# Kernel optimization log

Measured on AMD Instinct MI355X. Metric: run time of the kernel, lower is better.

The kernel has to match this reference:

```python
import jax, jax.numpy as jnp
import numpy as np

N_NODES = 100000
N_EDGES = 3200000
N_GRAPHS = 4096
N_REL = 5
N_BASES = 4
HID = 32


def setup_inputs() -> dict:
    key = jax.random.key(0)
    ks = jax.random.split(key, 32)
    inp = {}
    inp['x'] = jax.random.normal(ks[0], (N_NODES, 4), dtype=jnp.float32)
    inp['edge_index'] = jax.random.randint(ks[1], (2, N_EDGES), 0, N_NODES, dtype=jnp.int64)
    inp['edge_type'] = jax.random.randint(ks[2], (N_EDGES,), 0, N_REL, dtype=jnp.int64)
    inp['user_idx'] = jax.random.randint(ks[3], (N_GRAPHS,), 0, N_NODES, dtype=jnp.int64)
    inp['item_idx'] = jax.random.randint(ks[4], (N_GRAPHS,), 0, N_NODES, dtype=jnp.int64)
    k = 5
    for l in range(4):
        in_c = 4 if l == 0 else HID
        inp[f'basis{l}'] = jax.random.normal(ks[k], (N_BASES, in_c, HID), dtype=jnp.float32) * 0.1; k += 1
        inp[f'comp{l}'] = jax.random.normal(ks[k], (N_REL, N_BASES), dtype=jnp.float32) * 0.5; k += 1
        inp[f'root{l}'] = jax.random.normal(ks[k], (in_c, HID), dtype=jnp.float32) * 0.1; k += 1
        inp[f'bias{l}'] = jax.random.normal(ks[k], (HID,), dtype=jnp.float32) * 0.01; k += 1
    inp['w1'] = jax.random.normal(ks[k], (256, 128), dtype=jnp.float32) * 0.05; k += 1
    inp['b1'] = jnp.zeros((128,), dtype=jnp.float32)
    inp['w2'] = jax.random.normal(ks[k], (128, 1), dtype=jnp.float32) * 0.05; k += 1
    inp['b2'] = jnp.zeros((1,), dtype=jnp.float32)
    return inp


def _rgcn_layer(x, src, key5, inv_cnt, basis, comp, root, bias, n_nodes):
    # mean-aggregate raw source features per (dst, relation): [N, R, in]
    agg = jax.ops.segment_sum(x[src], key5, num_segments=n_nodes * N_REL)
    agg = agg.reshape(n_nodes, N_REL, -1) * inv_cnt
    # basis-decomposed relation weights: W_r = sum_b comp[r,b] * basis[b]
    w = jnp.einsum('rb,bio->rio', comp, basis)  # [R, in, out]
    return jnp.einsum('nri,rio->no', agg, w) + x @ root + bias


def reference(x, edge_index, edge_type, user_idx, item_idx,
              basis0, comp0, root0, bias0,
              basis1, comp1, root1, bias1,
              basis2, comp2, root2, bias2,
              basis3, comp3, root3, bias3,
              w1, b1, w2, b2):
    n_nodes = x.shape[0]
    src, dst = edge_index[0], edge_index[1]
    key5 = dst * N_REL + edge_type  # combined (dst, relation) segment id
    cnt = jax.ops.segment_sum(jnp.ones_like(edge_type, dtype=x.dtype), key5,
                              num_segments=n_nodes * N_REL)
    inv_cnt = (1.0 / jnp.maximum(cnt, 1.0)).reshape(n_nodes, N_REL, 1)
    params = [(basis0, comp0, root0, bias0), (basis1, comp1, root1, bias1),
              (basis2, comp2, root2, bias2), (basis3, comp3, root3, bias3)]
    out = x
    hs = []
    for (basis, comp, root, bias) in params:
        out = jnp.tanh(_rgcn_layer(out, src, key5, inv_cnt, basis, comp, root, bias, n_nodes))
        hs.append(out)
    h = jnp.concatenate(hs, axis=1)            # [N, 128]
    g = jnp.concatenate([h[user_idx], h[item_idx]], axis=1)  # [B, 256]
    z = jax.nn.relu(g @ w1 + b1)
    return (z @ w2 + b2)[:, 0]
```

## Files before the change

### kernel.cpp

```cpp
#include <hip/hip_runtime.h>
#include <hip/hip_bf16.h>
#include <hip/hip_fp16.h>

#define N_NODES 100000
#define N_EDGES 3200000
#define N_GRAPHS 4096
#define N_REL 5
#define N_BASES 4
#define HID 32
#define SEG (N_NODES*N_REL)
#define DUMMY N_NODES

#define NBUCK 392
#define BCAP  10240
#define PBCAP 15360
#define NKEY  1280
#define PTILE 4096

#define KDIM 192
#define ASTR 208

typedef _Float16 half8 __attribute__((ext_vector_type(8)));
typedef float floatx4 __attribute__((ext_vector_type(4)));

static __global__ __launch_bounds__(256) void k_part(const int* __restrict__ ei,
                                                     const int* __restrict__ et,
                                                     int* __restrict__ gcur,
                                                     unsigned long long* __restrict__ part) {
    __shared__ unsigned long long stage[PTILE];
    __shared__ int hist[NBUCK];
    __shared__ int lofs[NBUCK];
    __shared__ int lbase[NBUCK];
    __shared__ int sscan[256];
    int t = threadIdx.x;
    int e0 = blockIdx.x * PTILE;
    int tile_n = N_EDGES - e0; if (tile_n > PTILE) tile_n = PTILE;

    for (int k = t; k < NBUCK; k += 256) hist[k] = 0;
    __syncthreads();
    int src[16], bkt[16], lkey[16];
#pragma unroll
    for (int j = 0; j < 16; j++) {
        int e = e0 + j * 256 + t;
        if (e < N_EDGES) {
            int s = ei[e];
            int d = ei[N_EDGES + e];
            int r = et[e];
            src[j] = s; bkt[j] = d >> 8; lkey[j] = ((d & 255) * 5) + r;
            atomicAdd(&hist[bkt[j]], 1);
        } else bkt[j] = -1;
    }
    __syncthreads();
    int h0 = (2 * t     < NBUCK) ? hist[2 * t]     : 0;
    int h1 = (2 * t + 1 < NBUCK) ? hist[2 * t + 1] : 0;
    int s2 = h0 + h1;
    sscan[t] = s2;
    __syncthreads();
    for (int off = 1; off < 256; off <<= 1) {
        int xv = (t >= off) ? sscan[t - off] : 0;
        __syncthreads();
        sscan[t] += xv;
        __syncthreads();
    }
    int excl = sscan[t] - s2;
    if (2 * t     < NBUCK) lofs[2 * t]     = excl;
    if (2 * t + 1 < NBUCK) lofs[2 * t + 1] = excl + h0;
    for (int k = t; k < NBUCK; k += 256) lbase[k] = atomicAdd(&gcur[k], hist[k]);
    __syncthreads();
    for (int k = t; k < NBUCK; k += 256) hist[k] = 0;
    __syncthreads();
#pragma unroll
    for (int j = 0; j < 16; j++) {
        if (bkt[j] >= 0) {
            int rank = atomicAdd(&hist[bkt[j]], 1);
            stage[lofs[bkt[j]] + rank] =
                ((unsigned long long)(unsigned)((bkt[j] << 16) | lkey[j]) << 32)
                | (unsigned)src[j];
        }
    }
    __syncthreads();
    for (int i = t; i < tile_n; i += 256) {
        unsigned long long u = stage[i];
        unsigned hi = (unsigned)(u >> 32);
        int bb = hi >> 16;
        unsigned long long lk = hi & 0xFFFFu;
        int pos = lbase[bb] + (i - lofs[bb]);
        if (pos < BCAP)
            part[(size_t)bb * BCAP + pos] = (lk << 32) | (u & 0xffffffffULL);
    }
}

static __global__ __launch_bounds__(1024) void k_bsort(const unsigned long long* __restrict__ part,
                                                       const int* __restrict__ gcur,
                                                       int* __restrict__ offs,
                                                       int* __restrict__ cnt,
                                                       int* __restrict__ srcs) {
    __shared__ int lhist[NKEY];
    __shared__ int lscan[NKEY];
    __shared__ int sscan[256];
    __shared__ int lsrc[PBCAP];
    int b = blockIdx.x;
    int t = threadIdx.x;
    int n = gcur[b]; if (n > BCAP) n = BCAP;
    const unsigned long long* reg = part + (size_t)b * BCAP;

    for (int k = t; k < NKEY; k += 1024) lhist[k] = 0;
    __syncthreads();
    for (int i = t; i < n; i += 1024)
        atomicAdd(&lhist[(int)(reg[i] >> 32)], 1);
    __syncthreads();

    int loc[5]; int s5 = 0;
    if (t < 256) {
#pragma unroll
        for (int j = 0; j < 5; j++) { loc[j] = s5; s5 += (lhist[t * 5 + j] + 7) & ~7; }
        sscan[t] = s5;
    }
    __syncthreads();
    for (int off = 1; off < 256; off <<= 1) {
        int x = (t >= off && t < 256) ? sscan[t - off] : 0;
        __syncthreads();
        if (t < 256) sscan[t] += x;
        __syncthreads();
    }
    if (t < 256) {
        int excl = sscan[t] - s5;
#pragma unroll
        for (int j = 0; j < 5; j++) lscan[t * 5 + j] = excl + loc[j];
    }
    __syncthreads();
    int ptot = sscan[255]; if (ptot > PBCAP) ptot = PBCAP;
    int pout = ptot + 16; if (pout > PBCAP) pout = PBCAP;

    int base = b * PBCAP;
    if (t < 256) {
#pragma unroll
        for (int j = 0; j < 5; j++) {
            int k = t * 5 + j;
            int segid = b * NKEY + k;
            if (segid < SEG) {
                cnt[segid]  = lhist[k];
                offs[segid] = base + lscan[k];
            }
        }
    }
    __syncthreads();
    for (int k = t; k < NKEY; k += 1024) lhist[k] = 0;
    for (int i = t; i < pout; i += 1024) lsrc[i] = DUMMY;
    __syncthreads();
    for (int i = t; i < n; i += 1024) {
        unsigned long long u = reg[i];
        int k = (int)(u >> 32);
        int pos = lscan[k] + atomicAdd(&lhist[k], 1);
        if (pos < PBCAP) lsrc[pos] = (int)(u & 0xffffffffULL);
    }
    __syncthreads();
    for (int i = t; i < pout; i += 1024) srcs[base + i] = lsrc[i];
}

static __global__ __launch_bounds__(256) void k_prep(
    const float* __restrict__ x,
    __half* __restrict__ ht0, __half* __restrict__ ht1, __half* __restrict__ ht2,
    __half* __restrict__ ht3, __half* __restrict__ ht4, int* __restrict__ srcs,
    const float* __restrict__ ba0, const float* __restrict__ co0, const float* __restrict__ ro0,
    const float* __restrict__ ba1, const float* __restrict__ co1, const float* __restrict__ ro1,
    const float* __restrict__ ba2, const float* __restrict__ co2, const float* __restrict__ ro2,
    const float* __restrict__ ba3, const float* __restrict__ co3, const float* __restrict__ ro3,
    __half* __restrict__ Wb, const float* __restrict__ w1, __half* __restrict__ Wm) {
    int blk = blockIdx.x;
    int t = threadIdx.x;
    if (blk < 12501) {
        int tid = blk * 256 + t;
        if (tid < (N_NODES + 1) * 32) {
            int nd = tid >> 5, ii = tid & 31;
            float v = (nd < N_NODES && ii < 4) ? x[(nd << 2) + ii] : 0.f;
            ht0[tid] = __float2half(v);
        } else {
            int r = tid - (N_NODES + 1) * 32;
            if (r < 128) {
                __half* hp = (r < 32) ? ht1 : (r < 64) ? ht2 : (r < 96) ? ht3 : ht4;
                hp[N_NODES * 32 + (r & 31)] = __float2half(0.f);
            } else if (r < 144) srcs[NBUCK * PBCAP + (r - 128)] = DUMMY;
        }
    } else if (blk < 12501 + 96) {
        int idx = (blk - 12501) * 256 + t;
        int j    = idx & 7;
        int lane = (idx >> 3) & 63;
        int tile = (idx >> 9) & 1;
        int ls   = idx >> 10;
        int l    = ls / 6;
        int s    = ls - l * 6;
        const float* basis = (l == 0) ? ba0 : (l == 1) ? ba1 : (l == 2) ? ba2 : ba3;
        const float* comp  = (l == 0) ? co0 : (l == 1) ? co1 : (l == 2) ? co2 : co3;
        const float* root  = (l == 0) ? ro0 : (l == 1) ? ro1 : (l == 2) ? ro2 : ro3;
        int in_c = (l == 0) ? 4 : HID;
        int d = ((lane >> 4) << 3) + j;
        int o = tile * 16 + (lane & 15);
        float v = 0.f;
        if (d < in_c) {
            if (s < 5) {
                float acc = 0.f;
#pragma unroll
                for (int b = 0; b < N_BASES; b++)
                    acc += comp[s * N_BASES + b] * basis[(b * in_c + d) * HID + o];
                v = acc;
            } else {
                v = root[d * HID + o];
            }
        }
        Wb[idx] = __float2half(v);
    } else {
        int idx = (blk - 12597) * 256 + t;
        int j    = idx & 7;
        int lane = (idx >> 3) & 63;
        int s    = (idx >> 9) & 7;
        int tile = idx >> 12;
        int k = s * 32 + ((lane >> 4) << 3) + j;
        int o = tile * 16 + (lane & 15);
        Wm[idx] = __float2half(w1[k * 128 + o]);
    }
}

static __global__ __launch_bounds__(128, 5) void k_layer(
    const __half* __restrict__ tab, const int* __restrict__ offs,
    const int* __restrict__ cnt, const int* __restrict__ srcs,
    const __half* __restrict__ Wbl, const float* __restrict__ bias,
    __half* __restrict__ hout) {
    __shared__ __align__(16) __half sAgg[32 * ASTR];
    int t = threadIdx.x;
    int wave = t >> 6, lane = t & 63;
    int nsub = lane >> 2, cp = lane & 3;
    int nl = wave * 16 + nsub;
    int n = blockIdx.x * 32 + nl;
    const half8* tab8 = (const half8*)tab;

    int s5 = n * N_REL;
    int o0 = offs[s5];
    int cc[5];
#pragma unroll
    for (int r = 0; r < 5; r++) cc[r] = cnt[s5 + r];

    __half* row = sAgg + nl * ASTR;
    *(half8*)(row + 160 + cp * 8) = tab8[n * 4 + cp];

    int ob[5];
    {
        int orun = o0;
#pragma unroll
        for (int r = 0; r < 5; r++) { ob[r] = orun; orun += (cc[r] + 7) & ~7; }
    }
    int4 E0[5], E1[5];
#pragma unroll
    for (int r = 0; r < 5; r++) {
        const int* sp = srcs + ob[r];
        E0[r] = *(const int4*)(sp);
        E1[r] = *(const int4*)(sp + 4);
    }
#pragma unroll
    for (int r = 0; r < 5; r++) {
        int cr = cc[r];
        int pr = (cr + 7) & ~7;
        const int* sp = srcs + ob[r];
        half8 g0 = tab8[E0[r].x * 4 + cp], g1 = tab8[E0[r].y * 4 + cp];
        half8 g2 = tab8[E0[r].z * 4 + cp], g3 = tab8[E0[r].w * 4 + cp];
        half8 g4 = tab8[E1[r].x * 4 + cp], g5 = tab8[E1[r].y * 4 + cp];
        half8 g6 = tab8[E1[r].z * 4 + cp], g7 = tab8[E1[r].w * 4 + cp];
        half8 sb = ((g0 + g1) + (g2 + g3)) + ((g4 + g5) + (g6 + g7));
        float S0 = (float)sb[0], S1 = (float)sb[1], S2 = (float)sb[2], S3 = (float)sb[3];
        float S4 = (float)sb[4], S5 = (float)sb[5], S6 = (float)sb[6], S7 = (float)sb[7];
        for (int s8 = 8; s8 < pr; s8 += 8) {
            int4 f0 = *(const int4*)(sp + s8);
            int4 f1 = *(const int4*)(sp + s8 + 4);
            half8 h0 = tab8[f0.x * 4 + cp], h1 = tab8[f0.y * 4 + cp];
            half8 h2 = tab8[f0.z * 4 + cp], h3 = tab8[f0.w * 4 + cp];
            half8 h4 = tab8[f1.x * 4 + cp], h5 = tab8[f1.y * 4 + cp];
            half8 h6 = tab8[f1.z * 4 + cp], h7 = tab8[f1.w * 4 + cp];
            half8 rb = ((h0 + h1) + (h2 + h3)) + ((h4 + h5) + (h6 + h7));
            S0 += (float)rb[0]; S1 += (float)rb[1]; S2 += (float)rb[2]; S3 += (float)rb[3];
            S4 += (float)rb[4]; S5 += (float)rb[5]; S6 += (float)rb[6]; S7 += (float)rb[7];
        }
        float ic = (cr > 0) ? __builtin_amdgcn_rcpf((float)cr) : 0.f;
        half8 u;
        u[0] = (_Float16)(S0 * ic); u[1] = (_Float16)(S1 * ic);
        u[2] = (_Float16)(S2 * ic); u[3] = (_Float16)(S3 * ic);
        u[4] = (_Float16)(S4 * ic); u[5] = (_Float16)(S5 * ic);
        u[6] = (_Float16)(S6 * ic); u[7] = (_Float16)(S7 * ic);
        *(half8*)(row + r * 32 + cp * 8) = u;
    }
    __syncthreads();

    floatx4 acc0 = {0.f, 0.f, 0.f, 0.f}, acc1 = {0.f, 0.f, 0.f, 0.f};
    const __half* aBase = sAgg + (wave * 16 + (lane & 15)) * ASTR + ((lane >> 4) << 3);
    const __half* bBase = Wbl + lane * 8;
#pragma unroll
    for (int s = 0; s < 6; s++) {
        half8 a  = *(const half8*)(aBase + s * 32);
        half8 f0 = *(const half8*)(bBase + (s * 2 + 0) * 512);
        half8 f1 = *(const half8*)(bBase + (s * 2 + 1) * 512);
        acc0 = __builtin_amdgcn_mfma_f32_16x16x32_f16(a, f0, acc0, 0, 0, 0);
        acc1 = __builtin_amdgcn_mfma_f32_16x16x32_f16(a, f1, acc1, 0, 0, 0);
    }
    int oc = lane & 15;
    float bi0 = bias[oc], bi1 = bias[16 + oc];
#pragma unroll
    for (int r = 0; r < 4; r++) {
        int node = blockIdx.x * 32 + wave * 16 + ((lane >> 4) << 2) + r;
        hout[node * 32 + oc]      = __float2half(tanhf(acc0[r] + bi0));
        hout[node * 32 + 16 + oc] = __float2half(tanhf(acc1[r] + bi1));
    }
}

static __global__ __launch_bounds__(256) void k_mlp(
    const __half* __restrict__ h1, const __half* __restrict__ h2,
    const __half* __restrict__ h3, const __half* __restrict__ h4,
    const int* __restrict__ uidx, const int* __restrict__ iidx,
    const __half* __restrict__ Wm, const float* __restrict__ b1,
    const float* __restrict__ w2, const float* __restrict__ b2,
    float* __restrict__ out) {
    __shared__ __align__(16) __half sg[16 * 264];
    __shared__ float sacc[4][16];
    int t = threadIdx.x, wave = t >> 6, lane = t & 63;
    int g0 = blockIdx.x * 16;
    int lt = lane >> 4, lp = lane & 15;
    const __half* htab = (lt == 0) ? h1 : (lt == 1) ? h2 : (lt == 2) ? h3 : h4;
#pragma unroll
    for (int gg2 = 0; gg2 < 4; gg2++) {
        int gg = wave * 4 + gg2;
        int g = g0 + gg;
        int u = uidx[g], it = iidx[g];
        __half2* dst = (__half2*)(sg + gg * 264);
        dst[lt * 16 + lp]      = ((const __half2*)(htab + u * 32))[lp];
        dst[64 + lt * 16 + lp] = ((const __half2*)(htab + it * 32))[lp];
    }
    __syncthreads();
    floatx4 acc0 = {0.f, 0.f, 0.f, 0.f}, acc1 = {0.f, 0.f, 0.f, 0.f};
    const __half* aBase = sg + (lane & 15) * 264 + ((lane >> 4) << 3);
    const __half* bB0 = Wm + (wave * 2 + 0) * 4096 + lane * 8;
    const __half* bB1 = Wm + (wave * 2 + 1) * 4096 + lane * 8;
#pragma unroll
    for (int s = 0; s < 8; s++) {
        half8 a  = *(const half8*)(aBase + s * 32);
        half8 f0 = *(const half8*)(bB0 + s * 512);
        half8 f1 = *(const half8*)(bB1 + s * 512);
        acc0 = __builtin_amdgcn_mfma_f32_16x16x32_f16(a, f0, acc0, 0, 0, 0);
        acc1 = __builtin_amdgcn_mfma_f32_16x16x32_f16(a, f1, acc1, 0, 0, 0);
    }
    int o0 = wave * 32 + (lane & 15);
    int o1 = o0 + 16;
    float b10 = b1[o0], b11 = b1[o1], w20 = w2[o0], w21 = w2[o1];
#pragma unroll
    for (int r = 0; r < 4; r++) {
        float z0 = fmaxf(acc0[r] + b10, 0.f);
        float z1 = fmaxf(acc1[r] + b11, 0.f);
        float v = z0 * w20 + z1 * w21;
#pragma unroll
        for (int off = 1; off < 16; off <<= 1) v += __shfl_xor(v, off);
        if ((lane & 15) == 0) sacc[wave][((lane >> 4) << 2) + r] = v;
    }
    __syncthreads();
    if (t < 16)
        out[g0 + t] = sacc[0][t] + sacc[1][t] + sacc[2][t] + sacc[3][t] + b2[0];
}

extern "C" void kernel_launch(void* const* d_in, const int* in_sizes, int n_in,
                              void* d_out, int out_size, void* d_ws, size_t ws_size,
                              hipStream_t stream) {
    const float* x  = (const float*)d_in[0];
    const int*   ei = (const int*)d_in[1];
    const int*   et = (const int*)d_in[2];
    const int*   ui = (const int*)d_in[3];
    const int*   ii = (const int*)d_in[4];
    const float* w1 = (const float*)d_in[21];
    const float* b1 = (const float*)d_in[22];
    const float* w2 = (const float*)d_in[23];
    const float* b2 = (const float*)d_in[24];

    char* ws = (char*)d_ws;
    if (ws_size < 92167680UL) return;
    int*    gcur = (int*)(ws + 0);
    int*    offs = (int*)(ws + 2048);
    int*    cnt  = (int*)(ws + 2002176);
    int*    srcs = (int*)(ws + 4002304);
    __half* Wb   = (__half*)(ws + 28086912);
    __half* Wm   = (__half*)(ws + 28136064);
    __half* ht0  = (__half*)(ws + 28201600);
    __half* ht1  = (__half*)(ws + 34601728);
    __half* ht2  = (__half*)(ws + 41001856);
    __half* ht3  = (__half*)(ws + 47401984);
    __half* ht4  = (__half*)(ws + 53802112);
    unsigned long long* part = (unsigned long long*)(ws + 34601728);

    hipMemsetAsync(gcur, 0, NBUCK * 4, stream);

    k_part<<<(N_EDGES + PTILE - 1) / PTILE, 256, 0, stream>>>(ei, et, gcur, part);
    k_bsort<<<NBUCK, 1024, 0, stream>>>(part, gcur, offs, cnt, srcs);
    k_prep<<<12725, 256, 0, stream>>>(
        x, ht0, ht1, ht2, ht3, ht4, srcs,
        (const float*)d_in[5],  (const float*)d_in[6],  (const float*)d_in[7],
        (const float*)d_in[9],  (const float*)d_in[10], (const float*)d_in[11],
        (const float*)d_in[13], (const float*)d_in[14], (const float*)d_in[15],
        (const float*)d_in[17], (const float*)d_in[18], (const float*)d_in[19],
        Wb, w1, Wm);

    __half* tabs[5] = {ht0, ht1, ht2, ht3, ht4};
    for (int l = 0; l < 4; l++) {
        const float* bias = (const float*)d_in[8 + 4 * l];
        k_layer<<<N_NODES / 32, 128, 0, stream>>>(
            tabs[l], offs, cnt, srcs, Wb + l * 6144, bias, tabs[l + 1]);
    }
    k_mlp<<<256, 256, 0, stream>>>(ht1, ht2, ht3, ht4, ui, ii, Wm, b1, w2, b2,
                                   (float*)d_out);
}
```

Measured before the change: 335.5 us.

## Replace bucketed LDS partition sort with global atomic counting sort

```diff
diff --git a/kernel.cpp b/kernel.cpp
--- a/kernel.cpp
+++ b/kernel.cpp
@@ -8,14 +8,12 @@
 #define N_REL 5
 #define N_BASES 4
 #define HID 32
-#define SEG (N_NODES*N_REL)
+#define NKEYS (N_NODES*N_REL)
 #define DUMMY N_NODES
 
-#define NBUCK 392
-#define BCAP  10240
-#define PBCAP 15360
-#define NKEY  1280
-#define PTILE 4096
+#define SCANB 489
+#define SRCCAP 6803456
+#define FILLB 1661
 
 #define KDIM 192
 #define ASTR 208
@@ -23,145 +21,121 @@
 typedef _Float16 half8 __attribute__((ext_vector_type(8)));
 typedef float floatx4 __attribute__((ext_vector_type(4)));
 
-static __global__ __launch_bounds__(256) void k_part(const int* __restrict__ ei,
+static __global__ __launch_bounds__(256) void k_hist(const int* __restrict__ ei,
                                                      const int* __restrict__ et,
-                                                     int* __restrict__ gcur,
-                                                     unsigned long long* __restrict__ part) {
-    __shared__ unsigned long long stage[PTILE];
-    __shared__ int hist[NBUCK];
-    __shared__ int lofs[NBUCK];
-    __shared__ int lbase[NBUCK];
-    __shared__ int sscan[256];
-    int t = threadIdx.x;
-    int e0 = blockIdx.x * PTILE;
-    int tile_n = N_EDGES - e0; if (tile_n > PTILE) tile_n = PTILE;
-
-    for (int k = t; k < NBUCK; k += 256) hist[k] = 0;
-    __syncthreads();
-    int src[16], bkt[16], lkey[16];
-#pragma unroll
-    for (int j = 0; j < 16; j++) {
-        int e = e0 + j * 256 + t;
-        if (e < N_EDGES) {
-            int s = ei[e];
-            int d = ei[N_EDGES + e];
-            int r = et[e];
-            src[j] = s; bkt[j] = d >> 8; lkey[j] = ((d & 255) * 5) + r;
-            atomicAdd(&hist[bkt[j]], 1);
-        } else bkt[j] = -1;
-    }
-    __syncthreads();
-    int h0 = (2 * t     < NBUCK) ? hist[2 * t]     : 0;
-    int h1 = (2 * t + 1 < NBUCK) ? hist[2 * t + 1] : 0;
-    int s2 = h0 + h1;
-    sscan[t] = s2;
+                                                     int* __restrict__ cnt) {
+    int e = (blockIdx.x * 256 + threadIdx.x) * 4;
+    int4 d4 = *(const int4*)(ei + N_EDGES + e);
+    int4 r4 = *(const int4*)(et + e);
+    atomicAdd(&cnt[d4.x * 5 + r4.x], 1);
+    atomicAdd(&cnt[d4.y * 5 + r4.y], 1);
+    atomicAdd(&cnt[d4.z * 5 + r4.z], 1);
+    atomicAdd(&cnt[d4.w * 5 + r4.w], 1);
+}
+
+static __global__ __launch_bounds__(256) void k_scanA(const int* __restrict__ cnt,
+                                                      int* __restrict__ offs,
+                                                      int* __restrict__ bsum) {
+    __shared__ int ss[256];
+    int t = threadIdx.x;
+    int base = blockIdx.x * 1024 + t * 4;
+    int p0 = 0, p1 = 0, p2 = 0, p3 = 0;
+    if (base + 3 < NKEYS) {
+        int4 c = *(const int4*)(cnt + base);
+        p0 = (c.x + 7) & ~7; p1 = (c.y + 7) & ~7;
+        p2 = (c.z + 7) & ~7; p3 = (c.w + 7) & ~7;
+    } else {
+        if (base     < NKEYS) p0 = (cnt[base]     + 7) & ~7;
+        if (base + 1 < NKEYS) p1 = (cnt[base + 1] + 7) & ~7;
+        if (base + 2 < NKEYS) p2 = (cnt[base + 2] + 7) & ~7;
+        if (base + 3 < NKEYS) p3 = (cnt[base + 3] + 7) & ~7;
+    }
+    int s = p0 + p1 + p2 + p3;
+    ss[t] = s;
     __syncthreads();
     for (int off = 1; off < 256; off <<= 1) {
-        int xv = (t >= off) ? sscan[t - off] : 0;
+        int x = (t >= off) ? ss[t - off] : 0;
         __syncthreads();
-        sscan[t] += xv;
+        ss[t] += x;
         __syncthreads();
     }
-    int excl = sscan[t] - s2;
-    if (2 * t     < NBUCK) lofs[2 * t]     = excl;
-    if (2 * t + 1 < NBUCK) lofs[2 * t + 1] = excl + h0;
-    for (int k = t; k < NBUCK; k += 256) lbase[k] = atomicAdd(&gcur[k], hist[k]);
-    __syncthreads();
-    for (int k = t; k < NBUCK; k += 256) hist[k] = 0;
-    __syncthreads();
-#pragma unroll
-    for (int j = 0; j < 16; j++) {
-        if (bkt[j] >= 0) {
-            int rank = atomicAdd(&hist[bkt[j]], 1);
-            stage[lofs[bkt[j]] + rank] =
-                ((unsigned long long)(unsigned)((bkt[j] << 16) | lkey[j]) << 32)
-                | (unsigned)src[j];
+    int excl = ss[t] - s;
+    if (base     < NKEYS) offs[base]     = excl;
+    if (base + 1 < NKEYS) offs[base + 1] = excl + p0;
+    if (base + 2 < NKEYS) offs[base + 2] = excl + p0 + p1;
+    if (base + 3 < NKEYS) offs[base + 3] = excl + p0 + p1 + p2;
+    if (t == 255) bsum[blockIdx.x] = ss[255];
+}
+
+static __global__ __launch_bounds__(512) void k_scanB(int* __restrict__ bsum) {
+    __shared__ int ss[512];
+    int t = threadIdx.x;
+    int v = (t < SCANB) ? bsum[t] : 0;
+    ss[t] = v;
+    __syncthreads();
+    for (int off = 1; off < 512; off <<= 1) {
+        int x = (t >= off) ? ss[t - off] : 0;
+        __syncthreads();
+        ss[t] += x;
+        __syncthreads();
+    }
+    if (t < SCANB) bsum[t] = ss[t] - v;
+}
+
+static __global__ __launch_bounds__(256) void k_scanC(int* __restrict__ offs,
+                                                      const int* __restrict__ bsum,
+                                                      int* __restrict__ cur,
+                                                      int* __restrict__ srcs) {
+    int blk = blockIdx.x;
+    int t = threadIdx.x;
+    if (blk < SCANB) {
+        int bb = bsum[blk];
+        int base = blk * 1024 + t * 4;
+        if (base + 3 < NKEYS) {
+            int4 o = *(const int4*)(offs + base);
+            o.x += bb; o.y += bb; o.z += bb; o.w += bb;
+            *(int4*)(offs + base) = o;
+            *(int4*)(cur + base) = o;
+        } else {
+            for (int i = 0; i < 4; i++)
+                if (base + i < NKEYS) {
+                    int o = offs[base + i] + bb;
+                    offs[base + i] = o;
+                    cur[base + i] = o;
+                }
         }
-    }
-    __syncthreads();
-    for (int i = t; i < tile_n; i += 256) {
-        unsigned long long u = stage[i];
-        unsigned hi = (unsigned)(u >> 32);
-        int bb = hi >> 16;
-        unsigned long long lk = hi & 0xFFFFu;
-        int pos = lbase[bb] + (i - lofs[bb]);
-        if (pos < BCAP)
-            part[(size_t)bb * BCAP + pos] = (lk << 32) | (u & 0xffffffffULL);
-    }
-}
-
-static __global__ __launch_bounds__(1024) void k_bsort(const unsigned long long* __restrict__ part,
-                                                       const int* __restrict__ gcur,
-                                                       int* __restrict__ offs,
-                                                       int* __restrict__ cnt,
-                                                       int* __restrict__ srcs) {
-    __shared__ int lhist[NKEY];
-    __shared__ int lscan[NKEY];
-    __shared__ int sscan[256];
-    __shared__ int lsrc[PBCAP];
-    int b = blockIdx.x;
-    int t = threadIdx.x;
-    int n = gcur[b]; if (n > BCAP) n = BCAP;
-    const unsigned long long* reg = part + (size_t)b * BCAP;
-
-    for (int k = t; k < NKEY; k += 1024) lhist[k] = 0;
-    __syncthreads();
-    for (int i = t; i < n; i += 1024)
-        atomicAdd(&lhist[(int)(reg[i] >> 32)], 1);
-    __syncthreads();
-
-    int loc[5]; int s5 = 0;
-    if (t < 256) {
-#pragma unroll
-        for (int j = 0; j < 5; j++) { loc[j] = s5; s5 += (lhist[t * 5 + j] + 7) & ~7; }
-        sscan[t] = s5;
-    }
-    __syncthreads();
-    for (int off = 1; off < 256; off <<= 1) {
-        int x = (t >= off && t < 256) ? sscan[t - off] : 0;
-        __syncthreads();
-        if (t < 256) sscan[t] += x;
-        __syncthreads();
-    }
-    if (t < 256) {
-        int excl = sscan[t] - s5;
-#pragma unroll
-        for (int j = 0; j < 5; j++) lscan[t * 5 + j] = excl + loc[j];
-    }
-    __syncthreads();
-    int ptot = sscan[255]; if (ptot > PBCAP) ptot = PBCAP;
-    int pout = ptot + 16; if (pout > PBCAP) pout = PBCAP;
-
-    int base = b * PBCAP;
-    if (t < 256) {
-#pragma unroll
-        for (int j = 0; j < 5; j++) {
-            int k = t * 5 + j;
-            int segid = b * NKEY + k;
-            if (segid < SEG) {
-                cnt[segid]  = lhist[k];
-                offs[segid] = base + lscan[k];
-            }
-        }
-    }
-    __syncthreads();
-    for (int k = t; k < NKEY; k += 1024) lhist[k] = 0;
-    for (int i = t; i < pout; i += 1024) lsrc[i] = DUMMY;
-    __syncthreads();
-    for (int i = t; i < n; i += 1024) {
-        unsigned long long u = reg[i];
-        int k = (int)(u >> 32);
-        int pos = lscan[k] + atomicAdd(&lhist[k], 1);
-        if (pos < PBCAP) lsrc[pos] = (int)(u & 0xffffffffULL);
-    }
-    __syncthreads();
-    for (int i = t; i < pout; i += 1024) srcs[base + i] = lsrc[i];
+    } else {
+        int idx = (blk - SCANB) * 4096 + t * 16;
+        int4 dv; dv.x = dv.y = dv.z = dv.w = DUMMY;
+        *(int4*)(srcs + idx)      = dv;
+        *(int4*)(srcs + idx + 4)  = dv;
+        *(int4*)(srcs + idx + 8)  = dv;
+        *(int4*)(srcs + idx + 12) = dv;
+    }
+}
+
+static __global__ __launch_bounds__(256) void k_scatter(const int* __restrict__ ei,
+                                                        const int* __restrict__ et,
+                                                        int* __restrict__ cur,
+                                                        int* __restrict__ srcs) {
+    int e = (blockIdx.x * 256 + threadIdx.x) * 4;
+    int4 s4 = *(const int4*)(ei + e);
+    int4 d4 = *(const int4*)(ei + N_EDGES + e);
+    int4 r4 = *(const int4*)(et + e);
+    int p0 = atomicAdd(&cur[d4.x * 5 + r4.x], 1);
+    int p1 = atomicAdd(&cur[d4.y * 5 + r4.y], 1);
+    int p2 = atomicAdd(&cur[d4.z * 5 + r4.z], 1);
+    int p3 = atomicAdd(&cur[d4.w * 5 + r4.w], 1);
+    if (p0 < SRCCAP) srcs[p0] = s4.x;
+    if (p1 < SRCCAP) srcs[p1] = s4.y;
+    if (p2 < SRCCAP) srcs[p2] = s4.z;
+    if (p3 < SRCCAP) srcs[p3] = s4.w;
 }
 
 static __global__ __launch_bounds__(256) void k_prep(
     const float* __restrict__ x,
     __half* __restrict__ ht0, __half* __restrict__ ht1, __half* __restrict__ ht2,
-    __half* __restrict__ ht3, __half* __restrict__ ht4, int* __restrict__ srcs,
+    __half* __restrict__ ht3, __half* __restrict__ ht4,
     const float* __restrict__ ba0, const float* __restrict__ co0, const float* __restrict__ ro0,
     const float* __restrict__ ba1, const float* __restrict__ co1, const float* __restrict__ ro1,
     const float* __restrict__ ba2, const float* __restrict__ co2, const float* __restrict__ ro2,
@@ -180,7 +154,7 @@
             if (r < 128) {
                 __half* hp = (r < 32) ? ht1 : (r < 64) ? ht2 : (r < 96) ? ht3 : ht4;
                 hp[N_NODES * 32 + (r & 31)] = __float2half(0.f);
-            } else if (r < 144) srcs[NBUCK * PBCAP + (r - 128)] = DUMMY;
+            }
         }
     } else if (blk < 12501 + 96) {
         int idx = (blk - 12501) * 256 + t;
@@ -377,25 +351,28 @@
 
     char* ws = (char*)d_ws;
     if (ws_size < 92167680UL) return;
-    int*    gcur = (int*)(ws + 0);
-    int*    offs = (int*)(ws + 2048);
-    int*    cnt  = (int*)(ws + 2002176);
-    int*    srcs = (int*)(ws + 4002304);
-    __half* Wb   = (__half*)(ws + 28086912);
-    __half* Wm   = (__half*)(ws + 28136064);
-    __half* ht0  = (__half*)(ws + 28201600);
-    __half* ht1  = (__half*)(ws + 34601728);
-    __half* ht2  = (__half*)(ws + 41001856);
-    __half* ht3  = (__half*)(ws + 47401984);
-    __half* ht4  = (__half*)(ws + 53802112);
-    unsigned long long* part = (unsigned long long*)(ws + 34601728);
-
-    hipMemsetAsync(gcur, 0, NBUCK * 4, stream);
-
-    k_part<<<(N_EDGES + PTILE - 1) / PTILE, 256, 0, stream>>>(ei, et, gcur, part);
-    k_bsort<<<NBUCK, 1024, 0, stream>>>(part, gcur, offs, cnt, srcs);
+    int*    cnt  = (int*)(ws + 0);
+    int*    offs = (int*)(ws + 2000000);
+    int*    cur  = (int*)(ws + 4000000);
+    int*    bsum = (int*)(ws + 6000000);
+    int*    srcs = (int*)(ws + 6002048);
+    __half* Wb   = (__half*)(ws + 33215872);
+    __half* Wm   = (__half*)(ws + 33265024);
+    __half* ht0  = (__half*)(ws + 33330560);
+    __half* ht1  = (__half*)(ws + 39730688);
+    __half* ht2  = (__half*)(ws + 46130816);
+    __half* ht3  = (__half*)(ws + 52530944);
+    __half* ht4  = (__half*)(ws + 58931072);
+
+    hipMemsetAsync(cnt, 0, NKEYS * 4, stream);
+
+    k_hist<<<3125, 256, 0, stream>>>(ei, et, cnt);
+    k_scanA<<<SCANB, 256, 0, stream>>>(cnt, offs, bsum);
+    k_scanB<<<1, 512, 0, stream>>>(bsum);
+    k_scanC<<<SCANB + FILLB, 256, 0, stream>>>(offs, bsum, cur, srcs);
+    k_scatter<<<3125, 256, 0, stream>>>(ei, et, cur, srcs);
     k_prep<<<12725, 256, 0, stream>>>(
-        x, ht0, ht1, ht2, ht3, ht4, srcs,
+        x, ht0, ht1, ht2, ht3, ht4,
         (const float*)d_in[5],  (const float*)d_in[6],  (const float*)d_in[7],
         (const float*)d_in[9],  (const float*)d_in[10], (const float*)d_in[11],
         (const float*)d_in[13], (const float*)d_in[14], (const float*)d_in[15],
```

After: 685.5 us. 2.04x slower.
